# Optimization experiments

Measured on AMD Instinct MI355X. Metric: run time of the kernel, lower is better.

Reference implementation:

```python
import jax, jax.numpy as jnp
import numpy as np

E = 1024
H = 16
DH = E // H
EPS = 1e-8
GRAM_W = 1.5


def _gram_scores(q, k1, k2):
    # q: [BH, L, D], k1/k2: [BH, S, D] -> [BH, L, S]
    ll = jnp.sum(q * q, -1)[:, :, None]          # [BH, L, 1]
    vv = jnp.sum(k1 * k1, -1)[:, None, :]        # [BH, 1, S]
    aa = jnp.sum(k2 * k2, -1)[:, None, :]
    va = jnp.sum(k1 * k2, -1)[:, None, :]
    lv = jnp.einsum('bld,bsd->bls', q, k1)
    la = jnp.einsum('bld,bsd->bls', q, k2)
    det = ll * (vv * aa - va * va) - lv * (lv * aa - la * va) + la * (lv * va - la * vv)
    return -jnp.sqrt(jnp.clip(det, EPS, None))


def setup_inputs() -> dict:
    key = jax.random.key(0)
    ks = jax.random.split(key, 20)
    L, B, S = 512, 4, 1024
    inp = {
        'query': jax.random.normal(ks[0], (L, B, E), jnp.float32),
        'mod1': jax.random.normal(ks[1], (S, B, E), jnp.float32),
        'mod2': jax.random.normal(ks[2], (S, B, E), jnp.float32),
    }
    # Linear params stored as [in, out] (y = x @ W + b), 8 linears
    names = ['q', 'k1', 'k2', 'v1', 'v2', 'g1', 'g2', 'o']
    for i, n in enumerate(names):
        inp[n + '_w'] = jax.random.normal(ks[3 + 2 * i], (E, E), jnp.float32) * 0.02
        inp[n + '_b'] = jax.random.normal(ks[4 + 2 * i], (E,), jnp.float32) * 0.02
    return inp


def reference(query, mod1, mod2,
              q_w, q_b, k1_w, k1_b, k2_w, k2_b, v1_w, v1_b, v2_w, v2_b,
              g1_w, g1_b, g2_w, g2_b, o_w, o_b):
    L, B, _ = query.shape
    S = mod1.shape[0]
    scaling = DH ** -0.5

    def lin(x, w, b):
        return x @ w + b

    def split_heads(x, n):  # [n, B, E] -> [B*H, n, DH]
        return x.reshape(n, B * H, DH).transpose(1, 0, 2)

    q = split_heads(lin(query, q_w, q_b) * scaling, L)
    k1 = split_heads(lin(mod1, k1_w, k1_b), S)
    k2 = split_heads(lin(mod2, k2_w, k2_b), S)
    v1 = split_heads(lin(mod1, v1_w, v1_b), S)
    v2 = split_heads(lin(mod2, v2_w, v2_b), S)

    w1 = jnp.einsum('bld,bsd->bls', q, k1)
    w2 = jnp.einsum('bld,bsd->bls', q, k2)
    gram = _gram_scores(q, k1, k2)
    logits = GRAM_W * gram + w1 + w2          # [BH, L, S]
    attn = jax.nn.softmax(logits, axis=-1)

    def merge_heads(x):  # [B*H, L, DH] -> [L, B, E]
        return x.transpose(1, 0, 2).reshape(L, B, E)

    out1 = merge_heads(jnp.einsum('bls,bsd->bld', attn, v1))
    out2 = merge_heads(jnp.einsum('bls,bsd->bld', attn, v2))
    gate1 = jax.nn.sigmoid(lin(query, g1_w, g1_b))
    gate2 = jax.nn.sigmoid(lin(query, g2_w, g2_b))
    attn_output = lin((out1 * gate1 + out2 * gate2) / 2.0, o_w, o_b)
    avg_weights = attn.reshape(B, H, L, S).mean(axis=1)
    return attn_output, avg_weights
```

## Files before the change

kernel.cpp:

```cpp
#include <hip/hip_runtime.h>
#include <cstddef>
#include <cstdint>

typedef unsigned short ushort_t;
typedef unsigned int uint_t;
typedef __attribute__((ext_vector_type(8))) short short8;
typedef __attribute__((ext_vector_type(4))) float f32x4;

#define EDIM 1024
#define NHEAD 16
#define HDIM 64
#define NB 4
#define LQ 512
#define SK 1024
#define BHD 64

__device__ __forceinline__ ushort_t f2b(float f) {
    uint_t u = __float_as_uint(f);
    return (ushort_t)((u + 0x7fffu + ((u >> 16) & 1u)) >> 16);
}
__device__ __forceinline__ float b2f(ushort_t b) {
    return __uint_as_float(((uint_t)b) << 16);
}

__device__ __forceinline__ void gload_lds16(const void* g, void* l) {
    __builtin_amdgcn_global_load_lds((const __attribute__((address_space(1))) void*)g,
                                     (__attribute__((address_space(3))) void*)l, 16, 0, 0);
}

struct MegaArgs {
    const ushort_t *qx, *m1h, *m1l, *m2h, *m2l;
    const ushort_t *Wqg, *Wkv1, *Wkv2, *Wk1l, *Wk2l;
    const float *q_b, *k1_b, *k2_b, *v1_b, *v2_b, *g1_b, *g2_b;
    float *K1f, *K2f;
    ushort_t *V1b, *V2b, *Qb, *G1b, *G2b;
};

__global__ __launch_bounds__(256, 2)
void mega_gemm(MegaArgs a)
{
    __shared__ ushort_t As[128 * 64];
    __shared__ ushort_t Bs[128 * 64];
    const int tid = threadIdx.x;
    const int wave = tid >> 6, lane = tid & 63;
    const int ln = lane & 15, lq = lane >> 4;
    const int wm = wave & 1, wn = wave >> 1;
    const int cswz = (lane & 7) ^ ((lane >> 3) & 7);
    const int mrl = lane >> 3;

    const int id = blockIdx.x;
    const ushort_t *A, *Al, *B, *Bl;
    const float* bias;
    int npass, row0, col0, kind;
    if (id < 512) {
        kind = id >> 8;
        const int t = id & 255;
        col0 = (t & 7) * 128; row0 = (t >> 3) * 128; npass = 3;
        A = kind ? a.m2h : a.m1h;  Al = kind ? a.m2l : a.m1l;
        B = kind ? a.Wkv2 : a.Wkv1; Bl = kind ? a.Wk2l : a.Wk1l;
        bias = kind ? a.k2_b : a.k1_b;
    } else if (id < 1024) {
        int t = id - 512; kind = 2 + (t >> 8); t &= 255;
        col0 = (t & 7) * 128; row0 = (t >> 3) * 128; npass = 1;
        A = (kind == 2) ? a.m1h : a.m2h; Al = A;
        B = ((kind == 2) ? a.Wkv1 : a.Wkv2) + (size_t)1024 * 1024; Bl = B;
        bias = (kind == 2) ? a.v1_b : a.v2_b;
    } else {
        const int t = id - 1024; kind = 4;
        const int c = t % 24, rr = t / 24;
        col0 = c * 128; row0 = rr * 128; npass = 1;
        A = a.qx; Al = A; B = a.Wqg; Bl = B;
        const int seg = c >> 3;
        bias = (seg == 0) ? a.q_b : ((seg == 1) ? a.g1_b : a.g2_b);
    }

    f32x4 zero = {0.f, 0.f, 0.f, 0.f};
    f32x4 acc[4][4];
#pragma unroll
    for (int i = 0; i < 4; ++i)
#pragma unroll
        for (int j = 0; j < 4; ++j) acc[i][j] = zero;

    for (int pp = 0; pp < npass; ++pp) {
        const ushort_t* Ab = (pp == 2) ? Al : A;
        const ushort_t* Bb = (pp == 1) ? Bl : B;
        for (int kk = 0; kk < 1024; kk += 64) {
            __syncthreads();
#pragma unroll
            for (int j = 0; j < 4; ++j) {
                const int mr = (wave * 4 + j) * 8 + mrl;
                gload_lds16(Ab + (size_t)(row0 + mr) * 1024 + kk + cswz * 8,
                            (void*)(As + (wave * 4 + j) * 512));
                gload_lds16(Bb + (size_t)(col0 + mr) * 1024 + kk + cswz * 8,
                            (void*)(Bs + (wave * 4 + j) * 512));
            }
            __syncthreads();
#pragma unroll
            for (int sub = 0; sub < 2; ++sub) {
                short8 af[4], bfv[4];
#pragma unroll
                for (int i = 0; i < 4; ++i) {
                    const int ml = wm * 64 + i * 16 + ln;
                    af[i] = *(const short8*)(As + ml * 64 + (((sub * 4 + lq) ^ (ml & 7)) * 8));
                    const int nl = wn * 64 + i * 16 + ln;
                    bfv[i] = *(const short8*)(Bs + nl * 64 + (((sub * 4 + lq) ^ (nl & 7)) * 8));
                }
#pragma unroll
                for (int i = 0; i < 4; ++i)
#pragma unroll
                    for (int j = 0; j < 4; ++j)
                        acc[i][j] = __builtin_amdgcn_mfma_f32_16x16x32_bf16(af[i], bfv[j], acc[i][j], 0, 0, 0);
            }
        }
    }

#pragma unroll
    for (int i = 0; i < 4; ++i) {
#pragma unroll
        for (int r = 0; r < 4; ++r) {
            const int row = row0 + wm * 64 + i * 16 + lq * 4 + r;
#pragma unroll
            for (int j = 0; j < 4; ++j) {
                const int col = col0 + wn * 64 + j * 16 + ln;
                const int lc = col & 1023;
                float v = acc[i][j][r] + bias[lc];
                if (kind <= 1) {
                    const int s = row >> 2, b = row & 3, h = lc >> 6, d = lc & 63;
                    float* Y = kind ? a.K2f : a.K1f;
                    Y[(((size_t)(b * 16 + h)) * 1024 + s) * 64 + d] = v;
                } else if (kind <= 3) {
                    const int s = row >> 2, b = row & 3, h = lc >> 6, d = lc & 63;
                    ushort_t* Y = (kind == 2) ? a.V1b : a.V2b;
                    Y[(((size_t)(b * 16 + h)) * 1024 + s) * 64 + d] = f2b(v);
                } else {
                    const int seg = col >> 10;
                    if (seg == 0) {
                        v *= 0.125f;
                        const int s = row >> 2, b = row & 3, h = lc >> 6, d = lc & 63;
                        a.Qb[(((size_t)(b * 16 + h)) * 512 + s) * 64 + d] = f2b(v);
                    } else {
                        v = 1.0f / (1.0f + __expf(-v));
                        ushort_t* Y = (seg == 1) ? a.G1b : a.G2b;
                        Y[(size_t)row * 1024 + lc] = f2b(v);
                    }
                }
            }
        }
    }
}

struct CastArgs {
    const float* q; const float* m1; const float* m2;
    ushort_t* qx; ushort_t* m1h; ushort_t* m1l; ushort_t* m2h; ushort_t* m2l;
    const float* wsrc[8];
    ushort_t* whi[8];
    ushort_t* wlo[8];
};

__global__ __launch_bounds__(256)
void casts_kernel(CastArgs a)
{
    __shared__ float T[64][65];
    const int id = blockIdx.x;
    const int tid = threadIdx.x;
    if (id < 1024) {
        const size_t i = ((size_t)id * 256 + tid) * 8;
        float4 x = *(const float4*)(a.q + i);
        float4 y = *(const float4*)(a.q + i + 4);
        ushort_t o[8] = {f2b(x.x), f2b(x.y), f2b(x.z), f2b(x.w), f2b(y.x), f2b(y.y), f2b(y.z), f2b(y.w)};
        *(uint4*)( (void*)(a.qx + i) ) = *(const uint4*)o;
    } else if (id < 5120) {
        const int t = id - 1024;
        const int which = t >> 11;
        const float* x = which ? a.m2 : a.m1;
        ushort_t* yh = which ? a.m2h : a.m1h;
        ushort_t* yl = which ? a.m2l : a.m1l;
        const size_t i = ((size_t)(t & 2047) * 256 + tid) * 8;
        float v[8];
        *(float4*)v = *(const float4*)(x + i);
        *(float4*)(v + 4) = *(const float4*)(x + i + 4);
        ushort_t oh[8], ol[8];
#pragma unroll
        for (int k = 0; k < 8; ++k) {
            oh[k] = f2b(v[k]);
            ol[k] = f2b(v[k] - b2f(oh[k]));
        }
        *(uint4*)( (void*)(yh + i) ) = *(const uint4*)oh;
        *(uint4*)( (void*)(yl + i) ) = *(const uint4*)ol;
    } else {
        const int t = id - 5120;
        const int z = t >> 8, x = t & 15, y = (t >> 4) & 15;
        const float* W = a.wsrc[z];
        ushort_t* Th = a.whi[z];
        ushort_t* Tl = a.wlo[z];
        const int k0 = x * 64, n0 = y * 64;
        const int r = tid >> 2, cg = (tid & 3) * 16;
#pragma unroll
        for (int u = 0; u < 4; ++u) {
            float4 v = *(const float4*)(W + (size_t)(k0 + r) * 1024 + n0 + cg + u * 4);
            T[r][cg + u * 4 + 0] = v.x; T[r][cg + u * 4 + 1] = v.y;
            T[r][cg + u * 4 + 2] = v.z; T[r][cg + u * 4 + 3] = v.w;
        }
        __syncthreads();
        ushort_t oh[16], ol[16];
#pragma unroll
        for (int u = 0; u < 16; ++u) {
            float v = T[cg + u][r];
            oh[u] = f2b(v);
            ol[u] = f2b(v - b2f(oh[u]));
        }
        ushort_t* dh = Th + (size_t)(n0 + r) * 1024 + k0 + cg;
        *(uint4*)( (void*)dh ) = *(const uint4*)oh;
        *(uint4*)( (void*)(dh + 8) ) = *(const uint4*)(oh + 8);
        if (Tl) {
            ushort_t* dl = Tl + (size_t)(n0 + r) * 1024 + k0 + cg;
            *(uint4*)( (void*)dl ) = *(const uint4*)ol;
            *(uint4*)( (void*)(dl + 8) ) = *(const uint4*)(ol + 8);
        }
    }
}

__global__ __launch_bounds__(256)
void prep_kernel(const float* __restrict__ K1f, const float* __restrict__ K2f,
                 ushort_t* __restrict__ K1b, ushort_t* __restrict__ K2b,
                 float* __restrict__ vv, float* __restrict__ aa, float* __restrict__ va,
                 const ushort_t* __restrict__ Qb, float* __restrict__ ll,
                 const ushort_t* __restrict__ V1b, const ushort_t* __restrict__ V2b,
                 ushort_t* __restrict__ V1t, ushort_t* __restrict__ V2t)
{
    __shared__ float T[64][65];
    const int id = blockIdx.x;
    const int tid = threadIdx.x;
    const int wave = tid >> 6, lane = tid & 63;
    if (id < 16384) {
        const int row = id * 4 + wave;
        const float x1 = K1f[(size_t)row * 64 + lane];
        const float x2 = K2f[(size_t)row * 64 + lane];
        K1b[(size_t)row * 64 + lane] = f2b(x1);
        K2b[(size_t)row * 64 + lane] = f2b(x2);
        float s1 = x1 * x1, s2 = x2 * x2, s3 = x1 * x2;
#pragma unroll
        for (int o = 1; o < 64; o <<= 1) {
            s1 += __shfl_xor(s1, o);
            s2 += __shfl_xor(s2, o);
            s3 += __shfl_xor(s3, o);
        }
        if (lane == 0) { vv[row] = s1; aa[row] = s2; va[row] = s3; }
    } else if (id < 24576) {
        const int row = (id - 16384) * 4 + wave;
        const float x = b2f(Qb[(size_t)row * 64 + lane]);
        float s = x * x;
#pragma unroll
        for (int o = 1; o < 64; o <<= 1) s += __shfl_xor(s, o);
        if (lane == 0) ll[row] = s;
    } else {
        const int t = id - 24576;
        const int z = t >> 10, bh = (t >> 4) & 63, s0 = (t & 15) * 64;
        const ushort_t* S = z ? V2b : V1b;
        ushort_t* D = z ? V2t : V1t;
        const int r = tid >> 2, cg = (tid & 3) * 16;
        ushort_t buf[16];
        const ushort_t* sp = S + ((size_t)bh * 1024 + s0 + r) * 64 + cg;
        *(uint4*)buf = *(const uint4*)sp;
        *(uint4*)(buf + 8) = *(const uint4*)(sp + 8);
#pragma unroll
        for (int u = 0; u < 16; ++u) T[r][cg + u] = b2f(buf[u]);
        __syncthreads();
        ushort_t o[16];
#pragma unroll
        for (int u = 0; u < 16; ++u) o[u] = f2b(T[cg + u][r]);
        ushort_t* d = D + ((size_t)bh * 64 + r) * 1024 + s0 + cg;
        *(uint4*)( (void*)d ) = *(const uint4*)o;
        *(uint4*)( (void*)(d + 8) ) = *(const uint4*)(o + 8);
    }
}

__global__ __launch_bounds__(256, 2)
void scores_kernel(const ushort_t* __restrict__ Qb, const ushort_t* __restrict__ K1b,
                   const ushort_t* __restrict__ K2b, const float* __restrict__ ll,
                   const float* __restrict__ vv, const float* __restrict__ aa,
                   const float* __restrict__ va, float* __restrict__ logits)
{
    __shared__ ushort_t Qs[128 * 64];
    __shared__ ushort_t K1s[128 * 64];
    __shared__ ushort_t K2s[128 * 64];
    __shared__ float llS[128], vvS[128], aaS[128], vaS[128];
    const int tid = threadIdx.x;
    const int wave = tid >> 6, lane = tid & 63;
    const int ln = lane & 15, lq = lane >> 4;
    const int wm = wave & 1, wn = wave >> 1;
    const int bh = blockIdx.z;
    const int l0 = blockIdx.y * 128, s0 = blockIdx.x * 128;
    const int cswz = (lane & 7) ^ ((lane >> 3) & 7);
    const int mrl = lane >> 3;

    if (tid < 128) {
        llS[tid] = ll[(size_t)bh * 512 + l0 + tid];
        vvS[tid] = vv[(size_t)bh * 1024 + s0 + tid];
        aaS[tid] = aa[(size_t)bh * 1024 + s0 + tid];
        vaS[tid] = va[(size_t)bh * 1024 + s0 + tid];
    }
#pragma unroll
    for (int j = 0; j < 4; ++j) {
        const int mr = (wave * 4 + j) * 8 + mrl;
        gload_lds16(Qb + ((size_t)bh * 512 + l0 + mr) * 64 + cswz * 8, (void*)(Qs + (wave * 4 + j) * 512));
        gload_lds16(K1b + ((size_t)bh * 1024 + s0 + mr) * 64 + cswz * 8, (void*)(K1s + (wave * 4 + j) * 512));
        gload_lds16(K2b + ((size_t)bh * 1024 + s0 + mr) * 64 + cswz * 8, (void*)(K2s + (wave * 4 + j) * 512));
    }
    __syncthreads();

    f32x4 zero = {0.f, 0.f, 0.f, 0.f};
    f32x4 lv[4][4], la[4][4];
#pragma unroll
    for (int i = 0; i < 4; ++i)
#pragma unroll
        for (int j = 0; j < 4; ++j) { lv[i][j] = zero; la[i][j] = zero; }

#pragma unroll
    for (int sub = 0; sub < 2; ++sub) {
        short8 qf[4], k1f[4], k2f[4];
#pragma unroll
        for (int i = 0; i < 4; ++i) {
            const int ml = wm * 64 + i * 16 + ln;
            qf[i] = *(const short8*)(Qs + ml * 64 + (((sub * 4 + lq) ^ (ml & 7)) * 8));
            const int nl = wn * 64 + i * 16 + ln;
            k1f[i] = *(const short8*)(K1s + nl * 64 + (((sub * 4 + lq) ^ (nl & 7)) * 8));
            k2f[i] = *(const short8*)(K2s + nl * 64 + (((sub * 4 + lq) ^ (nl & 7)) * 8));
        }
#pragma unroll
        for (int i = 0; i < 4; ++i)
#pragma unroll
            for (int j = 0; j < 4; ++j) {
                lv[i][j] = __builtin_amdgcn_mfma_f32_16x16x32_bf16(qf[i], k1f[j], lv[i][j], 0, 0, 0);
                la[i][j] = __builtin_amdgcn_mfma_f32_16x16x32_bf16(qf[i], k2f[j], la[i][j], 0, 0, 0);
            }
    }

#pragma unroll
    for (int i = 0; i < 4; ++i) {
#pragma unroll
        for (int r = 0; r < 4; ++r) {
            const int l_loc = wm * 64 + i * 16 + lq * 4 + r;
            const float LL = llS[l_loc];
#pragma unroll
            for (int j = 0; j < 4; ++j) {
                const int s_loc = wn * 64 + j * 16 + ln;
                const float VV = vvS[s_loc], AA = aaS[s_loc], VA = vaS[s_loc];
                const float LV = lv[i][j][r], LA = la[i][j][r];
                float det = LL * (VV * AA - VA * VA) - LV * (LV * AA - LA * VA) + LA * (LV * VA - LA * VV);
                det = fmaxf(det, 1e-8f);
                logits[((size_t)bh * 512 + l0 + l_loc) * 1024 + s0 + s_loc] = LV + LA - 1.5f * sqrtf(det);
            }
        }
    }
}

__global__ __launch_bounds__(256)
void softmax_avg_kernel(float* __restrict__ logits, float* __restrict__ avg)
{
    __shared__ float part[4][1024];
    const int b = blockIdx.x >> 9, l = blockIdx.x & 511;
    const int wave = threadIdx.x >> 6, lane = threadIdx.x & 63;
    float pacc[16];
#pragma unroll
    for (int u = 0; u < 16; ++u) pacc[u] = 0.f;
#pragma unroll
    for (int jj = 0; jj < 4; ++jj) {
        const int h = wave * 4 + jj;
        float* rowp = logits + (((size_t)(b * 16 + h)) * 512 + l) * 1024;
        float4 v[4];
#pragma unroll
        for (int c = 0; c < 4; ++c) v[c] = *(const float4*)(rowp + c * 256 + lane * 4);
        float m = -3.4e38f;
#pragma unroll
        for (int c = 0; c < 4; ++c) m = fmaxf(m, fmaxf(fmaxf(v[c].x, v[c].y), fmaxf(v[c].z, v[c].w)));
#pragma unroll
        for (int o = 1; o < 64; o <<= 1) m = fmaxf(m, __shfl_xor(m, o));
        float s = 0.f;
#pragma unroll
        for (int c = 0; c < 4; ++c) {
            v[c].x = __expf(v[c].x - m); v[c].y = __expf(v[c].y - m);
            v[c].z = __expf(v[c].z - m); v[c].w = __expf(v[c].w - m);
            s += v[c].x + v[c].y + v[c].z + v[c].w;
        }
#pragma unroll
        for (int o = 1; o < 64; o <<= 1) s += __shfl_xor(s, o);
        const float inv = 1.0f / s;
        ushort_t* arow = (ushort_t*)rowp;
#pragma unroll
        for (int c = 0; c < 4; ++c) {
            const float p0 = v[c].x * inv, p1 = v[c].y * inv, p2 = v[c].z * inv, p3 = v[c].w * inv;
            ushort_t w[4] = {f2b(p0), f2b(p1), f2b(p2), f2b(p3)};
            *(uint2*)( (void*)(arow + c * 256 + lane * 4) ) = *(const uint2*)w;
            pacc[c * 4 + 0] += p0; pacc[c * 4 + 1] += p1;
            pacc[c * 4 + 2] += p2; pacc[c * 4 + 3] += p3;
        }
    }
#pragma unroll
    for (int c = 0; c < 4; ++c) {
        float4 pv = {pacc[c * 4 + 0], pacc[c * 4 + 1], pacc[c * 4 + 2], pacc[c * 4 + 3]};
        *(float4*)(&part[wave][c * 256 + lane * 4]) = pv;
    }
    __syncthreads();
    const int s0 = threadIdx.x * 4;
    float4 a0 = *(const float4*)(&part[0][s0]);
    float4 a1 = *(const float4*)(&part[1][s0]);
    float4 a2 = *(const float4*)(&part[2][s0]);
    float4 a3 = *(const float4*)(&part[3][s0]);
    float4 o;
    o.x = (a0.x + a1.x + a2.x + a3.x) * 0.0625f;
    o.y = (a0.y + a1.y + a2.y + a3.y) * 0.0625f;
    o.z = (a0.z + a1.z + a2.z + a3.z) * 0.0625f;
    o.w = (a0.w + a1.w + a2.w + a3.w) * 0.0625f;
    *(float4*)(avg + ((size_t)(b * 512 + l)) * 1024 + s0) = o;
}

__global__ __launch_bounds__(256, 2)
void pv_gate_kernel(const ushort_t* __restrict__ attn, const ushort_t* __restrict__ V1t,
                    const ushort_t* __restrict__ V2t, const ushort_t* __restrict__ G1,
                    const ushort_t* __restrict__ G2, ushort_t* __restrict__ tmpb)
{
    __shared__ ushort_t Ps[128 * 64];
    __shared__ ushort_t V1s[64 * 64];
    __shared__ ushort_t V2s[64 * 64];
    const int tid = threadIdx.x;
    const int wave = tid >> 6, lane = tid & 63;
    const int ln = lane & 15, lq = lane >> 4;
    const int bh = blockIdx.y;
    const int l0 = blockIdx.x * 128;
    const int cswz = (lane & 7) ^ ((lane >> 3) & 7);
    const int mrl = lane >> 3;
    const int bq = bh >> 4, h = bh & 15;

    f32x4 zero = {0.f, 0.f, 0.f, 0.f};
    f32x4 acc1[2][4], acc2[2][4];
#pragma unroll
    for (int i = 0; i < 2; ++i)
#pragma unroll
        for (int j = 0; j < 4; ++j) { acc1[i][j] = zero; acc2[i][j] = zero; }

    for (int s0 = 0; s0 < 1024; s0 += 64) {
        __syncthreads();
#pragma unroll
        for (int j = 0; j < 4; ++j) {
            const int mr = (wave * 4 + j) * 8 + mrl;
            gload_lds16(attn + ((size_t)bh * 512 + l0 + mr) * 2048 + s0 + cswz * 8,
                        (void*)(Ps + (wave * 4 + j) * 512));
        }
#pragma unroll
        for (int j = 0; j < 2; ++j) {
            const int mv = (wave * 2 + j) * 8 + mrl;
            gload_lds16(V1t + ((size_t)bh * 64 + mv) * 1024 + s0 + cswz * 8,
                        (void*)(V1s + (wave * 2 + j) * 512));
            gload_lds16(V2t + ((size_t)bh * 64 + mv) * 1024 + s0 + cswz * 8,
                        (void*)(V2s + (wave * 2 + j) * 512));
        }
        __syncthreads();
#pragma unroll
        for (int sub = 0; sub < 2; ++sub) {
            short8 af[2], b1f[4], b2f_[4];
#pragma unroll
            for (int i = 0; i < 2; ++i) {
                const int ml = wave * 32 + i * 16 + ln;
                af[i] = *(const short8*)(Ps + ml * 64 + (((sub * 4 + lq) ^ (ml & 7)) * 8));
            }
#pragma unroll
            for (int j = 0; j < 4; ++j) {
                const int nl = j * 16 + ln;
                b1f[j] = *(const short8*)(V1s + nl * 64 + (((sub * 4 + lq) ^ (nl & 7)) * 8));
                b2f_[j] = *(const short8*)(V2s + nl * 64 + (((sub * 4 + lq) ^ (nl & 7)) * 8));
            }
#pragma unroll
            for (int i = 0; i < 2; ++i)
#pragma unroll
                for (int j = 0; j < 4; ++j) {
                    acc1[i][j] = __builtin_amdgcn_mfma_f32_16x16x32_bf16(af[i], b1f[j], acc1[i][j], 0, 0, 0);
                    acc2[i][j] = __builtin_amdgcn_mfma_f32_16x16x32_bf16(af[i], b2f_[j], acc2[i][j], 0, 0, 0);
                }
        }
    }

#pragma unroll
    for (int i = 0; i < 2; ++i) {
#pragma unroll
        for (int r = 0; r < 4; ++r) {
            const int l = l0 + wave * 32 + i * 16 + lq * 4 + r;
#pragma unroll
            for (int j = 0; j < 4; ++j) {
                const int d = j * 16 + ln;
                const size_t addr = ((size_t)l * 4 + bq) * 1024 + h * 64 + d;
                const float v = 0.5f * (acc1[i][j][r] * b2f(G1[addr]) + acc2[i][j][r] * b2f(G2[addr]));
                tmpb[addr] = f2b(v);
            }
        }
    }
}

__global__ __launch_bounds__(256, 2)
void gemm_o64(const ushort_t* __restrict__ A, const ushort_t* __restrict__ B,
              const float* __restrict__ bias, float* __restrict__ Y)
{
    __shared__ ushort_t As[64 * 64];
    __shared__ ushort_t Bs[128 * 64];
    const int tid = threadIdx.x;
    const int wave = tid >> 6, lane = tid & 63;
    const int ln = lane & 15, lq = lane >> 4;
    const int row0 = blockIdx.y * 64, col0 = blockIdx.x * 128;
    const int wm = wave & 1, wn = wave >> 1;
    const int cswz = (lane & 7) ^ ((lane >> 3) & 7);
    const int mrl = lane >> 3;

    f32x4 zero = {0.f, 0.f, 0.f, 0.f};
    f32x4 acc[2][4];
#pragma unroll
    for (int i = 0; i < 2; ++i)
#pragma unroll
        for (int j = 0; j < 4; ++j) acc[i][j] = zero;

    for (int kk = 0; kk < 1024; kk += 64) {
        __syncthreads();
#pragma unroll
        for (int j = 0; j < 2; ++j) {
            const int mr = (wave * 2 + j) * 8 + mrl;
            gload_lds16(A + (size_t)(row0 + mr) * 1024 + kk + cswz * 8,
                        (void*)(As + (wave * 2 + j) * 512));
        }
#pragma unroll
        for (int j = 0; j < 4; ++j) {
            const int mr = (wave * 4 + j) * 8 + mrl;
            gload_lds16(B + (size_t)(col0 + mr) * 1024 + kk + cswz * 8,
                        (void*)(Bs + (wave * 4 + j) * 512));
        }
        __syncthreads();
#pragma unroll
        for (int sub = 0; sub < 2; ++sub) {
            short8 af[2], bfv[4];
#pragma unroll
            for (int i = 0; i < 2; ++i) {
                const int ml = wm * 32 + i * 16 + ln;
                af[i] = *(const short8*)(As + ml * 64 + (((sub * 4 + lq) ^ (ml & 7)) * 8));
            }
#pragma unroll
            for (int j = 0; j < 4; ++j) {
                const int nl = wn * 64 + j * 16 + ln;
                bfv[j] = *(const short8*)(Bs + nl * 64 + (((sub * 4 + lq) ^ (nl & 7)) * 8));
            }
#pragma unroll
            for (int i = 0; i < 2; ++i)
#pragma unroll
                for (int j = 0; j < 4; ++j)
                    acc[i][j] = __builtin_amdgcn_mfma_f32_16x16x32_bf16(af[i], bfv[j], acc[i][j], 0, 0, 0);
        }
    }

#pragma unroll
    for (int i = 0; i < 2; ++i) {
#pragma unroll
        for (int r = 0; r < 4; ++r) {
            const int row = row0 + wm * 32 + i * 16 + lq * 4 + r;
#pragma unroll
            for (int j = 0; j < 4; ++j) {
                const int col = col0 + wn * 64 + j * 16 + ln;
                Y[(size_t)row * 1024 + col] = acc[i][j][r] + bias[col];
            }
        }
    }
}

extern "C" void kernel_launch(void* const* d_in, const int* in_sizes, int n_in,
                              void* d_out, int out_size, void* d_ws, size_t ws_size,
                              hipStream_t stream)
{
    const float* query = (const float*)d_in[0];
    const float* mod1  = (const float*)d_in[1];
    const float* mod2  = (const float*)d_in[2];
    const float* q_w  = (const float*)d_in[3];  const float* q_b  = (const float*)d_in[4];
    const float* k1_w = (const float*)d_in[5];  const float* k1_b = (const float*)d_in[6];
    const float* k2_w = (const float*)d_in[7];  const float* k2_b = (const float*)d_in[8];
    const float* v1_w = (const float*)d_in[9];  const float* v1_b = (const float*)d_in[10];
    const float* v2_w = (const float*)d_in[11]; const float* v2_b = (const float*)d_in[12];
    const float* g1_w = (const float*)d_in[13]; const float* g1_b = (const float*)d_in[14];
    const float* g2_w = (const float*)d_in[15]; const float* g2_b = (const float*)d_in[16];
    const float* o_w  = (const float*)d_in[17]; const float* o_b  = (const float*)d_in[18];
    float* out = (float*)d_out;

    const size_t MB = 1u << 20;
    char* w = (char*)d_ws;
    ushort_t* Wqg  = (ushort_t*)(w + 0 * MB);
    ushort_t* Wkv1 = (ushort_t*)(w + 6 * MB);
    ushort_t* Wkv2 = (ushort_t*)(w + 10 * MB);
    ushort_t* Wo   = (ushort_t*)(w + 14 * MB);
    ushort_t* Wk1l = (ushort_t*)(w + 16 * MB);
    ushort_t* Wk2l = (ushort_t*)(w + 18 * MB);
    ushort_t* qx   = (ushort_t*)(w + 20 * MB);
    ushort_t* tmpb = qx;
    ushort_t* Qb   = (ushort_t*)(w + 24 * MB);
    ushort_t* K1b  = (ushort_t*)(w + 28 * MB);
    ushort_t* K2b  = (ushort_t*)(w + 36 * MB);
    ushort_t* V1t  = (ushort_t*)(w + 44 * MB);
    ushort_t* V2t  = (ushort_t*)(w + 52 * MB);
    ushort_t* G1b  = (ushort_t*)(w + 60 * MB);
    ushort_t* G2b  = (ushort_t*)(w + 64 * MB);
    float* ll = (float*)(w + 68 * MB);
    float* vv = (float*)(w + 68 * MB + 256 * 1024);
    float* aa = (float*)(w + 68 * MB + 512 * 1024);
    float* va = (float*)(w + 68 * MB + 768 * 1024);
    float* logits = (float*)(w + 78 * MB);
    ushort_t* m1h = (ushort_t*)(w + 78 * MB);
    ushort_t* m2h = (ushort_t*)(w + 86 * MB);
    ushort_t* m1l = (ushort_t*)(w + 94 * MB);
    ushort_t* m2l = (ushort_t*)(w + 102 * MB);
    float* K1f = (float*)(w + 110 * MB);
    float* K2f = (float*)(w + 126 * MB);
    ushort_t* V1b = (ushort_t*)(w + 142 * MB);
    ushort_t* V2b = (ushort_t*)(w + 150 * MB);
    ushort_t* attn = (ushort_t*)logits;

    CastArgs ca;
    ca.q = query; ca.m1 = mod1; ca.m2 = mod2;
    ca.qx = qx; ca.m1h = m1h; ca.m1l = m1l; ca.m2h = m2h; ca.m2l = m2l;
    const float* srcs[8] = {q_w, g1_w, g2_w, k1_w, v1_w, k2_w, v2_w, o_w};
    ushort_t* his[8] = {Wqg, Wqg + (size_t)1024 * 1024, Wqg + (size_t)2048 * 1024,
                        Wkv1, Wkv1 + (size_t)1024 * 1024, Wkv2, Wkv2 + (size_t)1024 * 1024, Wo};
    ushort_t* los[8] = {nullptr, nullptr, nullptr, Wk1l, nullptr, Wk2l, nullptr, nullptr};
    for (int i = 0; i < 8; ++i) { ca.wsrc[i] = srcs[i]; ca.whi[i] = his[i]; ca.wlo[i] = los[i]; }
    casts_kernel<<<7168, 256, 0, stream>>>(ca);

    MegaArgs ma;
    ma.qx = qx; ma.m1h = m1h; ma.m1l = m1l; ma.m2h = m2h; ma.m2l = m2l;
    ma.Wqg = Wqg; ma.Wkv1 = Wkv1; ma.Wkv2 = Wkv2; ma.Wk1l = Wk1l; ma.Wk2l = Wk2l;
    ma.q_b = q_b; ma.k1_b = k1_b; ma.k2_b = k2_b; ma.v1_b = v1_b; ma.v2_b = v2_b;
    ma.g1_b = g1_b; ma.g2_b = g2_b;
    ma.K1f = K1f; ma.K2f = K2f; ma.V1b = V1b; ma.V2b = V2b;
    ma.Qb = Qb; ma.G1b = G1b; ma.G2b = G2b;
    mega_gemm<<<1408, 256, 0, stream>>>(ma);

    prep_kernel<<<26624, 256, 0, stream>>>(K1f, K2f, K1b, K2b, vv, aa, va,
                                           Qb, ll, V1b, V2b, V1t, V2t);

    scores_kernel<<<dim3(8, 4, 64), 256, 0, stream>>>(Qb, K1b, K2b, ll, vv, aa, va, logits);
    softmax_avg_kernel<<<2048, 256, 0, stream>>>(logits, out + (size_t)LQ * NB * EDIM);
    pv_gate_kernel<<<dim3(4, 64), 256, 0, stream>>>(attn, V1t, V2t, G1b, G2b, tmpb);
    gemm_o64<<<dim3(8, 32), 256, 0, stream>>>(tmpb, Wo, o_b, out);
}
```

Before: 397.4 us.

## Fuse scores, softmax and PV-gate into a two-pass flash-attention kernel

Replaces the separate scores, softmax/average and PV-gate kernels with one two-pass kernel per (128-row query tile, batch-head). The first pass computes the Gram-augmented logits and running row max/sum; the second recomputes the logits, writes normalized bf16 probabilities to the attention buffer and accumulates P·V1/P·V2 with gating in registers. A small kernel then averages the bf16 probabilities over heads. This avoids writing and re-reading the fp32 logits tensor, at the cost of computing QK twice, only 256 blocks of 512 threads, and per-tile barriers for the row reductions.

Result: slower. 444.0 us (+11.7%).

```diff
diff --git a/kernel.cpp b/kernel.cpp
--- a/kernel.cpp
+++ b/kernel.cpp
@@ -275,225 +275,274 @@
     }
 }
 
-__global__ __launch_bounds__(256, 2)
-void scores_kernel(const ushort_t* __restrict__ Qb, const ushort_t* __restrict__ K1b,
-                   const ushort_t* __restrict__ K2b, const float* __restrict__ ll,
-                   const float* __restrict__ vv, const float* __restrict__ aa,
-                   const float* __restrict__ va, float* __restrict__ logits)
+__global__ __launch_bounds__(512, 1)
+void flash_attn(const ushort_t* __restrict__ Qb, const ushort_t* __restrict__ K1b,
+                const ushort_t* __restrict__ K2b, const ushort_t* __restrict__ V1t,
+                const ushort_t* __restrict__ V2t, const float* __restrict__ ll,
+                const float* __restrict__ vv, const float* __restrict__ aa,
+                const float* __restrict__ va, const ushort_t* __restrict__ G1,
+                const ushort_t* __restrict__ G2, ushort_t* __restrict__ attn,
+                ushort_t* __restrict__ tmpb)
 {
     __shared__ ushort_t Qs[128 * 64];
     __shared__ ushort_t K1s[128 * 64];
     __shared__ ushort_t K2s[128 * 64];
-    __shared__ float llS[128], vvS[128], aaS[128], vaS[128];
+    __shared__ ushort_t V1s[64 * 128];
+    __shared__ ushort_t V2s[64 * 128];
+    __shared__ ushort_t Ps[128 * 128];
+    __shared__ float vvS[1024], aaS[1024], vaS[1024];
+    __shared__ float llS[128], mRow[128], sRow[128];
+    __shared__ float redM[256], redS[256];
+
     const int tid = threadIdx.x;
     const int wave = tid >> 6, lane = tid & 63;
     const int ln = lane & 15, lq = lane >> 4;
-    const int wm = wave & 1, wn = wave >> 1;
-    const int bh = blockIdx.z;
-    const int l0 = blockIdx.y * 128, s0 = blockIdx.x * 128;
-    const int cswz = (lane & 7) ^ ((lane >> 3) & 7);
-    const int mrl = lane >> 3;
-
+    const int wm = wave >> 1, wn = wave & 1;
+    const int l0 = blockIdx.x * 128;
+    const int bh = blockIdx.y;
+    const int bq = bh >> 4, h = bh & 15;
+
+    for (int u = tid; u < 1024; u += 512) {
+        vvS[u] = vv[(size_t)bh * 1024 + u];
+        aaS[u] = aa[(size_t)bh * 1024 + u];
+        vaS[u] = va[(size_t)bh * 1024 + u];
+    }
     if (tid < 128) {
         llS[tid] = ll[(size_t)bh * 512 + l0 + tid];
-        vvS[tid] = vv[(size_t)bh * 1024 + s0 + tid];
-        aaS[tid] = aa[(size_t)bh * 1024 + s0 + tid];
-        vaS[tid] = va[(size_t)bh * 1024 + s0 + tid];
-    }
-#pragma unroll
-    for (int j = 0; j < 4; ++j) {
-        const int mr = (wave * 4 + j) * 8 + mrl;
-        gload_lds16(Qb + ((size_t)bh * 512 + l0 + mr) * 64 + cswz * 8, (void*)(Qs + (wave * 4 + j) * 512));
-        gload_lds16(K1b + ((size_t)bh * 1024 + s0 + mr) * 64 + cswz * 8, (void*)(K1s + (wave * 4 + j) * 512));
-        gload_lds16(K2b + ((size_t)bh * 1024 + s0 + mr) * 64 + cswz * 8, (void*)(K2s + (wave * 4 + j) * 512));
+        mRow[tid] = -3.4e38f;
+        sRow[tid] = 0.f;
+    }
+#pragma unroll
+    for (int c = 0; c < 2; ++c) {
+        const int row = wave * 16 + c * 8 + (lane >> 3);
+        const int ch = (lane & 7) ^ (row & 7);
+        gload_lds16(Qb + ((size_t)bh * 512 + l0 + row) * 64 + ch * 8,
+                    (void*)(Qs + (wave * 16 + c * 8) * 64));
     }
     __syncthreads();
 
     f32x4 zero = {0.f, 0.f, 0.f, 0.f};
-    f32x4 lv[4][4], la[4][4];
-#pragma unroll
-    for (int i = 0; i < 4; ++i)
-#pragma unroll
-        for (int j = 0; j < 4; ++j) { lv[i][j] = zero; la[i][j] = zero; }
-
-#pragma unroll
-    for (int sub = 0; sub < 2; ++sub) {
-        short8 qf[4], k1f[4], k2f[4];
-#pragma unroll
-        for (int i = 0; i < 4; ++i) {
-            const int ml = wm * 64 + i * 16 + ln;
-            qf[i] = *(const short8*)(Qs + ml * 64 + (((sub * 4 + lq) ^ (ml & 7)) * 8));
-            const int nl = wn * 64 + i * 16 + ln;
-            k1f[i] = *(const short8*)(K1s + nl * 64 + (((sub * 4 + lq) ^ (nl & 7)) * 8));
-            k2f[i] = *(const short8*)(K2s + nl * 64 + (((sub * 4 + lq) ^ (nl & 7)) * 8));
-        }
-#pragma unroll
-        for (int i = 0; i < 4; ++i)
-#pragma unroll
-            for (int j = 0; j < 4; ++j) {
-                lv[i][j] = __builtin_amdgcn_mfma_f32_16x16x32_bf16(qf[i], k1f[j], lv[i][j], 0, 0, 0);
-                la[i][j] = __builtin_amdgcn_mfma_f32_16x16x32_bf16(qf[i], k2f[j], la[i][j], 0, 0, 0);
-            }
-    }
-
-#pragma unroll
-    for (int i = 0; i < 4; ++i) {
+
+    for (int st = 0; st < 8; ++st) {
+        const int s0 = st * 128;
+        __syncthreads();
+#pragma unroll
+        for (int c = 0; c < 2; ++c) {
+            const int row = wave * 16 + c * 8 + (lane >> 3);
+            const int ch = (lane & 7) ^ (row & 7);
+            gload_lds16(K1b + ((size_t)bh * 1024 + s0 + row) * 64 + ch * 8,
+                        (void*)(K1s + (wave * 16 + c * 8) * 64));
+            gload_lds16(K2b + ((size_t)bh * 1024 + s0 + row) * 64 + ch * 8,
+                        (void*)(K2s + (wave * 16 + c * 8) * 64));
+        }
+        __syncthreads();
+
+        f32x4 lv[2][4], la[2][4];
+#pragma unroll
+        for (int i = 0; i < 2; ++i)
+#pragma unroll
+            for (int j = 0; j < 4; ++j) { lv[i][j] = zero; la[i][j] = zero; }
+#pragma unroll
+        for (int sub = 0; sub < 2; ++sub) {
+            short8 qf[2], k1f[4], k2f[4];
+#pragma unroll
+            for (int i = 0; i < 2; ++i) {
+                const int ml = wm * 32 + i * 16 + ln;
+                qf[i] = *(const short8*)(Qs + ml * 64 + (((sub * 4 + lq) ^ (ml & 7)) * 8));
+            }
+#pragma unroll
+            for (int j = 0; j < 4; ++j) {
+                const int nl = wn * 64 + j * 16 + ln;
+                k1f[j] = *(const short8*)(K1s + nl * 64 + (((sub * 4 + lq) ^ (nl & 7)) * 8));
+                k2f[j] = *(const short8*)(K2s + nl * 64 + (((sub * 4 + lq) ^ (nl & 7)) * 8));
+            }
+#pragma unroll
+            for (int i = 0; i < 2; ++i)
+#pragma unroll
+                for (int j = 0; j < 4; ++j) {
+                    lv[i][j] = __builtin_amdgcn_mfma_f32_16x16x32_bf16(qf[i], k1f[j], lv[i][j], 0, 0, 0);
+                    la[i][j] = __builtin_amdgcn_mfma_f32_16x16x32_bf16(qf[i], k2f[j], la[i][j], 0, 0, 0);
+                }
+        }
+#pragma unroll
+        for (int i = 0; i < 2; ++i)
+#pragma unroll
+            for (int j = 0; j < 4; ++j) {
+                const int s_loc = wn * 64 + j * 16 + ln;
+                const float VV = vvS[s0 + s_loc], AA = aaS[s0 + s_loc], VA = vaS[s0 + s_loc];
+#pragma unroll
+                for (int r = 0; r < 4; ++r) {
+                    const float LL = llS[wm * 32 + i * 16 + lq * 4 + r];
+                    const float LV = lv[i][j][r], LA = la[i][j][r];
+                    float det = LL * (VV * AA - VA * VA) - LV * (LV * AA - LA * VA) + LA * (LV * VA - LA * VV);
+                    det = fmaxf(det, 1e-8f);
+                    lv[i][j][r] = LV + LA - 1.5f * sqrtf(det);
+                }
+            }
+#pragma unroll
+        for (int i = 0; i < 2; ++i)
+#pragma unroll
+            for (int r = 0; r < 4; ++r) {
+                float m = fmaxf(fmaxf(lv[i][0][r], lv[i][1][r]), fmaxf(lv[i][2][r], lv[i][3][r]));
+#pragma unroll
+                for (int o = 1; o < 16; o <<= 1) m = fmaxf(m, __shfl_xor(m, o));
+                if (ln == 0) redM[wn * 128 + wm * 32 + i * 16 + lq * 4 + r] = m;
+            }
+        __syncthreads();
+        if (tid < 128) {
+            const float mo = mRow[tid];
+            const float mn = fmaxf(mo, fmaxf(redM[tid], redM[128 + tid]));
+            sRow[tid] *= __expf(mo - mn);
+            mRow[tid] = mn;
+        }
+        __syncthreads();
+#pragma unroll
+        for (int i = 0; i < 2; ++i)
+#pragma unroll
+            for (int r = 0; r < 4; ++r) {
+                const float mr = mRow[wm * 32 + i * 16 + lq * 4 + r];
+                float e = __expf(lv[i][0][r] - mr) + __expf(lv[i][1][r] - mr)
+                        + __expf(lv[i][2][r] - mr) + __expf(lv[i][3][r] - mr);
+#pragma unroll
+                for (int o = 1; o < 16; o <<= 1) e += __shfl_xor(e, o);
+                if (ln == 0) redS[wn * 128 + wm * 32 + i * 16 + lq * 4 + r] = e;
+            }
+        __syncthreads();
+        if (tid < 128) sRow[tid] += redS[tid] + redS[128 + tid];
+    }
+    __syncthreads();
+    if (tid < 128) sRow[tid] = 1.0f / sRow[tid];
+
+    f32x4 o1[4], o2[4];
+#pragma unroll
+    for (int j = 0; j < 4; ++j) { o1[j] = zero; o2[j] = zero; }
+
+    for (int st = 0; st < 8; ++st) {
+        const int s0 = st * 128;
+        __syncthreads();
+#pragma unroll
+        for (int c = 0; c < 2; ++c) {
+            const int row = wave * 16 + c * 8 + (lane >> 3);
+            const int ch = (lane & 7) ^ (row & 7);
+            gload_lds16(K1b + ((size_t)bh * 1024 + s0 + row) * 64 + ch * 8,
+                        (void*)(K1s + (wave * 16 + c * 8) * 64));
+            gload_lds16(K2b + ((size_t)bh * 1024 + s0 + row) * 64 + ch * 8,
+                        (void*)(K2s + (wave * 16 + c * 8) * 64));
+        }
+#pragma unroll
+        for (int c = 0; c < 2; ++c) {
+            const int dr = wave * 8 + c * 4 + (lane >> 4);
+            const int ch = (lane & 15) ^ (dr & 7);
+            gload_lds16(V1t + ((size_t)bh * 64 + dr) * 1024 + s0 + ch * 8,
+                        (void*)(V1s + (wave * 8 + c * 4) * 128));
+            gload_lds16(V2t + ((size_t)bh * 64 + dr) * 1024 + s0 + ch * 8,
+                        (void*)(V2s + (wave * 8 + c * 4) * 128));
+        }
+        __syncthreads();
+
+        f32x4 lv[2][4], la[2][4];
+#pragma unroll
+        for (int i = 0; i < 2; ++i)
+#pragma unroll
+            for (int j = 0; j < 4; ++j) { lv[i][j] = zero; la[i][j] = zero; }
+#pragma unroll
+        for (int sub = 0; sub < 2; ++sub) {
+            short8 qf[2], k1f[4], k2f[4];
+#pragma unroll
+            for (int i = 0; i < 2; ++i) {
+                const int ml = wm * 32 + i * 16 + ln;
+                qf[i] = *(const short8*)(Qs + ml * 64 + (((sub * 4 + lq) ^ (ml & 7)) * 8));
+            }
+#pragma unroll
+            for (int j = 0; j < 4; ++j) {
+                const int nl = wn * 64 + j * 16 + ln;
+                k1f[j] = *(const short8*)(K1s + nl * 64 + (((sub * 4 + lq) ^ (nl & 7)) * 8));
+                k2f[j] = *(const short8*)(K2s + nl * 64 + (((sub * 4 + lq) ^ (nl & 7)) * 8));
+            }
+#pragma unroll
+            for (int i = 0; i < 2; ++i)
+#pragma unroll
+                for (int j = 0; j < 4; ++j) {
+                    lv[i][j] = __builtin_amdgcn_mfma_f32_16x16x32_bf16(qf[i], k1f[j], lv[i][j], 0, 0, 0);
+                    la[i][j] = __builtin_amdgcn_mfma_f32_16x16x32_bf16(qf[i], k2f[j], la[i][j], 0, 0, 0);
+                }
+        }
+#pragma unroll
+        for (int i = 0; i < 2; ++i)
+#pragma unroll
+            for (int j = 0; j < 4; ++j) {
+                const int s_loc = wn * 64 + j * 16 + ln;
+                const float VV = vvS[s0 + s_loc], AA = aaS[s0 + s_loc], VA = vaS[s0 + s_loc];
+#pragma unroll
+                for (int r = 0; r < 4; ++r) {
+                    const int l_loc = wm * 32 + i * 16 + lq * 4 + r;
+                    const float LL = llS[l_loc];
+                    const float LV = lv[i][j][r], LA = la[i][j][r];
+                    float det = LL * (VV * AA - VA * VA) - LV * (LV * AA - LA * VA) + LA * (LV * VA - LA * VV);
+                    det = fmaxf(det, 1e-8f);
+                    const float lg = LV + LA - 1.5f * sqrtf(det);
+                    const float p = __expf(lg - mRow[l_loc]) * sRow[l_loc];
+                    Ps[l_loc * 128 + (((s_loc >> 3) ^ (l_loc & 7)) * 8) + (s_loc & 7)] = f2b(p);
+                }
+            }
+        __syncthreads();
+#pragma unroll
+        for (int it = 0; it < 4; ++it) {
+            const int l = it * 32 + (tid >> 4);
+            const int c = tid & 15;
+            uint4 val = *(const uint4*)(Ps + l * 128 + ((c ^ (l & 7)) * 8));
+            *(uint4*)( (void*)(attn + ((size_t)bh * 512 + l0 + l) * 1024 + s0 + c * 8) ) = val;
+        }
+#pragma unroll
+        for (int kt = 0; kt < 4; ++kt) {
+            const int lA = wave * 16 + ln;
+            short8 pf = *(const short8*)(Ps + lA * 128 + (((kt * 4 + lq) ^ (lA & 7)) * 8));
+#pragma unroll
+            for (int j = 0; j < 4; ++j) {
+                const int d = j * 16 + ln;
+                short8 v1f = *(const short8*)(V1s + d * 128 + (((kt * 4 + lq) ^ (d & 7)) * 8));
+                short8 v2f = *(const short8*)(V2s + d * 128 + (((kt * 4 + lq) ^ (d & 7)) * 8));
+                o1[j] = __builtin_amdgcn_mfma_f32_16x16x32_bf16(pf, v1f, o1[j], 0, 0, 0);
+                o2[j] = __builtin_amdgcn_mfma_f32_16x16x32_bf16(pf, v2f, o2[j], 0, 0, 0);
+            }
+        }
+    }
+#pragma unroll
+    for (int j = 0; j < 4; ++j)
 #pragma unroll
         for (int r = 0; r < 4; ++r) {
-            const int l_loc = wm * 64 + i * 16 + lq * 4 + r;
-            const float LL = llS[l_loc];
-#pragma unroll
-            for (int j = 0; j < 4; ++j) {
-                const int s_loc = wn * 64 + j * 16 + ln;
-                const float VV = vvS[s_loc], AA = aaS[s_loc], VA = vaS[s_loc];
-                const float LV = lv[i][j][r], LA = la[i][j][r];
-                float det = LL * (VV * AA - VA * VA) - LV * (LV * AA - LA * VA) + LA * (LV * VA - LA * VV);
-                det = fmaxf(det, 1e-8f);
-                logits[((size_t)bh * 512 + l0 + l_loc) * 1024 + s0 + s_loc] = LV + LA - 1.5f * sqrtf(det);
-            }
-        }
-    }
+            const int l = l0 + wave * 16 + lq * 4 + r;
+            const int d = j * 16 + ln;
+            const size_t addr = ((size_t)l * 4 + bq) * 1024 + h * 64 + d;
+            const float v = 0.5f * (o1[j][r] * b2f(G1[addr]) + o2[j][r] * b2f(G2[addr]));
+            tmpb[addr] = f2b(v);
+        }
 }
 
 __global__ __launch_bounds__(256)
-void softmax_avg_kernel(float* __restrict__ logits, float* __restrict__ avg)
+void head_avg_kernel(const ushort_t* __restrict__ attn, float* __restrict__ outv)
 {
-    __shared__ float part[4][1024];
-    const int b = blockIdx.x >> 9, l = blockIdx.x & 511;
-    const int wave = threadIdx.x >> 6, lane = threadIdx.x & 63;
-    float pacc[16];
-#pragma unroll
-    for (int u = 0; u < 16; ++u) pacc[u] = 0.f;
-#pragma unroll
-    for (int jj = 0; jj < 4; ++jj) {
-        const int h = wave * 4 + jj;
-        float* rowp = logits + (((size_t)(b * 16 + h)) * 512 + l) * 1024;
-        float4 v[4];
-#pragma unroll
-        for (int c = 0; c < 4; ++c) v[c] = *(const float4*)(rowp + c * 256 + lane * 4);
-        float m = -3.4e38f;
-#pragma unroll
-        for (int c = 0; c < 4; ++c) m = fmaxf(m, fmaxf(fmaxf(v[c].x, v[c].y), fmaxf(v[c].z, v[c].w)));
-#pragma unroll
-        for (int o = 1; o < 64; o <<= 1) m = fmaxf(m, __shfl_xor(m, o));
-        float s = 0.f;
-#pragma unroll
-        for (int c = 0; c < 4; ++c) {
-            v[c].x = __expf(v[c].x - m); v[c].y = __expf(v[c].y - m);
-            v[c].z = __expf(v[c].z - m); v[c].w = __expf(v[c].w - m);
-            s += v[c].x + v[c].y + v[c].z + v[c].w;
-        }
-#pragma unroll
-        for (int o = 1; o < 64; o <<= 1) s += __shfl_xor(s, o);
-        const float inv = 1.0f / s;
-        ushort_t* arow = (ushort_t*)rowp;
-#pragma unroll
-        for (int c = 0; c < 4; ++c) {
-            const float p0 = v[c].x * inv, p1 = v[c].y * inv, p2 = v[c].z * inv, p3 = v[c].w * inv;
-            ushort_t w[4] = {f2b(p0), f2b(p1), f2b(p2), f2b(p3)};
-            *(uint2*)( (void*)(arow + c * 256 + lane * 4) ) = *(const uint2*)w;
-            pacc[c * 4 + 0] += p0; pacc[c * 4 + 1] += p1;
-            pacc[c * 4 + 2] += p2; pacc[c * 4 + 3] += p3;
-        }
-    }
-#pragma unroll
-    for (int c = 0; c < 4; ++c) {
-        float4 pv = {pacc[c * 4 + 0], pacc[c * 4 + 1], pacc[c * 4 + 2], pacc[c * 4 + 3]};
-        *(float4*)(&part[wave][c * 256 + lane * 4]) = pv;
-    }
-    __syncthreads();
-    const int s0 = threadIdx.x * 4;
-    float4 a0 = *(const float4*)(&part[0][s0]);
-    float4 a1 = *(const float4*)(&part[1][s0]);
-    float4 a2 = *(const float4*)(&part[2][s0]);
-    float4 a3 = *(const float4*)(&part[3][s0]);
-    float4 o;
-    o.x = (a0.x + a1.x + a2.x + a3.x) * 0.0625f;
-    o.y = (a0.y + a1.y + a2.y + a3.y) * 0.0625f;
-    o.z = (a0.z + a1.z + a2.z + a3.z) * 0.0625f;
-    o.w = (a0.w + a1.w + a2.w + a3.w) * 0.0625f;
-    *(float4*)(avg + ((size_t)(b * 512 + l)) * 1024 + s0) = o;
-}
-
-__global__ __launch_bounds__(256, 2)
-void pv_gate_kernel(const ushort_t* __restrict__ attn, const ushort_t* __restrict__ V1t,
-                    const ushort_t* __restrict__ V2t, const ushort_t* __restrict__ G1,
-                    const ushort_t* __restrict__ G2, ushort_t* __restrict__ tmpb)
-{
-    __shared__ ushort_t Ps[128 * 64];
-    __shared__ ushort_t V1s[64 * 64];
-    __shared__ ushort_t V2s[64 * 64];
-    const int tid = threadIdx.x;
-    const int wave = tid >> 6, lane = tid & 63;
-    const int ln = lane & 15, lq = lane >> 4;
-    const int bh = blockIdx.y;
-    const int l0 = blockIdx.x * 128;
-    const int cswz = (lane & 7) ^ ((lane >> 3) & 7);
-    const int mrl = lane >> 3;
-    const int bq = bh >> 4, h = bh & 15;
-
-    f32x4 zero = {0.f, 0.f, 0.f, 0.f};
-    f32x4 acc1[2][4], acc2[2][4];
-#pragma unroll
-    for (int i = 0; i < 2; ++i)
-#pragma unroll
-        for (int j = 0; j < 4; ++j) { acc1[i][j] = zero; acc2[i][j] = zero; }
-
-    for (int s0 = 0; s0 < 1024; s0 += 64) {
-        __syncthreads();
-#pragma unroll
-        for (int j = 0; j < 4; ++j) {
-            const int mr = (wave * 4 + j) * 8 + mrl;
-            gload_lds16(attn + ((size_t)bh * 512 + l0 + mr) * 2048 + s0 + cswz * 8,
-                        (void*)(Ps + (wave * 4 + j) * 512));
-        }
-#pragma unroll
-        for (int j = 0; j < 2; ++j) {
-            const int mv = (wave * 2 + j) * 8 + mrl;
-            gload_lds16(V1t + ((size_t)bh * 64 + mv) * 1024 + s0 + cswz * 8,
-                        (void*)(V1s + (wave * 2 + j) * 512));
-            gload_lds16(V2t + ((size_t)bh * 64 + mv) * 1024 + s0 + cswz * 8,
-                        (void*)(V2s + (wave * 2 + j) * 512));
-        }
-        __syncthreads();
-#pragma unroll
-        for (int sub = 0; sub < 2; ++sub) {
-            short8 af[2], b1f[4], b2f_[4];
-#pragma unroll
-            for (int i = 0; i < 2; ++i) {
-                const int ml = wave * 32 + i * 16 + ln;
-                af[i] = *(const short8*)(Ps + ml * 64 + (((sub * 4 + lq) ^ (ml & 7)) * 8));
-            }
-#pragma unroll
-            for (int j = 0; j < 4; ++j) {
-                const int nl = j * 16 + ln;
-                b1f[j] = *(const short8*)(V1s + nl * 64 + (((sub * 4 + lq) ^ (nl & 7)) * 8));
-                b2f_[j] = *(const short8*)(V2s + nl * 64 + (((sub * 4 + lq) ^ (nl & 7)) * 8));
-            }
-#pragma unroll
-            for (int i = 0; i < 2; ++i)
-#pragma unroll
-                for (int j = 0; j < 4; ++j) {
-                    acc1[i][j] = __builtin_amdgcn_mfma_f32_16x16x32_bf16(af[i], b1f[j], acc1[i][j], 0, 0, 0);
-                    acc2[i][j] = __builtin_amdgcn_mfma_f32_16x16x32_bf16(af[i], b2f_[j], acc2[i][j], 0, 0, 0);
-                }
-        }
-    }
-
-#pragma unroll
-    for (int i = 0; i < 2; ++i) {
-#pragma unroll
-        for (int r = 0; r < 4; ++r) {
-            const int l = l0 + wave * 32 + i * 16 + lq * 4 + r;
-#pragma unroll
-            for (int j = 0; j < 4; ++j) {
-                const int d = j * 16 + ln;
-                const size_t addr = ((size_t)l * 4 + bq) * 1024 + h * 64 + d;
-                const float v = 0.5f * (acc1[i][j][r] * b2f(G1[addr]) + acc2[i][j][r] * b2f(G2[addr]));
-                tmpb[addr] = f2b(v);
-            }
-        }
-    }
+    const int idx = blockIdx.x * 256 + threadIdx.x;
+    const int s8 = idx & 127;
+    const int l = (idx >> 7) & 511;
+    const int b = idx >> 16;
+    float acc[8] = {};
+#pragma unroll
+    for (int h = 0; h < 16; ++h) {
+        const ushort_t* p = attn + (((size_t)(b * 16 + h) * 512 + l)) * 1024 + s8 * 8;
+        uint4 u = *(const uint4*)p;
+        const uint_t uu[4] = {u.x, u.y, u.z, u.w};
+#pragma unroll
+        for (int q = 0; q < 4; ++q) {
+            acc[2 * q]     += __uint_as_float((uu[q] & 0xffffu) << 16);
+            acc[2 * q + 1] += __uint_as_float(uu[q] & 0xffff0000u);
+        }
+    }
+    float* d = outv + (size_t)idx * 8;
+    float4 o1 = {acc[0] * 0.0625f, acc[1] * 0.0625f, acc[2] * 0.0625f, acc[3] * 0.0625f};
+    float4 o2 = {acc[4] * 0.0625f, acc[5] * 0.0625f, acc[6] * 0.0625f, acc[7] * 0.0625f};
+    *(float4*)d = o1;
+    *(float4*)(d + 4) = o2;
 }
 
 __global__ __launch_bounds__(256, 2)
@@ -605,7 +654,7 @@
     float* vv = (float*)(w + 68 * MB + 256 * 1024);
     float* aa = (float*)(w + 68 * MB + 512 * 1024);
     float* va = (float*)(w + 68 * MB + 768 * 1024);
-    float* logits = (float*)(w + 78 * MB);
+    ushort_t* attn = (ushort_t*)(w + 78 * MB);
     ushort_t* m1h = (ushort_t*)(w + 78 * MB);
     ushort_t* m2h = (ushort_t*)(w + 86 * MB);
     ushort_t* m1l = (ushort_t*)(w + 94 * MB);
@@ -614,7 +663,6 @@
     float* K2f = (float*)(w + 126 * MB);
     ushort_t* V1b = (ushort_t*)(w + 142 * MB);
     ushort_t* V2b = (ushort_t*)(w + 150 * MB);
-    ushort_t* attn = (ushort_t*)logits;
 
     CastArgs ca;
     ca.q = query; ca.m1 = mod1; ca.m2 = mod2;
@@ -638,8 +686,9 @@
     prep_kernel<<<26624, 256, 0, stream>>>(K1f, K2f, K1b, K2b, vv, aa, va,
                                            Qb, ll, V1b, V2b, V1t, V2t);
 
-    scores_kernel<<<dim3(8, 4, 64), 256, 0, stream>>>(Qb, K1b, K2b, ll, vv, aa, va, logits);
-    softmax_avg_kernel<<<2048, 256, 0, stream>>>(logits, out + (size_t)LQ * NB * EDIM);
-    pv_gate_kernel<<<dim3(4, 64), 256, 0, stream>>>(attn, V1t, V2t, G1b, G2b, tmpb);
+    flash_attn<<<dim3(4, 64), 512, 0, stream>>>(Qb, K1b, K2b, V1t, V2t,
+                                                ll, vv, aa, va, G1b, G2b, attn, tmpb);
+
+    head_avg_kernel<<<1024, 256, 0, stream>>>(attn, out + (size_t)LQ * NB * EDIM);
     gemm_o64<<<dim3(8, 32), 256, 0, stream>>>(tmpb, Wo, o_b, out);
 }
```
